# Optimization experiments

Measured on AMD Instinct MI355X. Metric: run time of the kernel, lower is better.

## Reference

```python
import jax, jax.numpy as jnp
import numpy as np

B, T, D, H = 256, 1024, 64, 128


def _orthogonal(key, shape):
    a = jax.random.normal(key, (max(shape), max(shape)), dtype=jnp.float32)
    q, _ = jnp.linalg.qr(a)
    return q[: shape[0], : shape[1]].astype(jnp.float32)


def setup_inputs() -> dict:
    key = jax.random.key(0)
    k0, k1, k2, k3 = jax.random.split(key, 4)
    x = jax.random.normal(k0, (B, T, D), dtype=jnp.float32)
    W_xK = _orthogonal(k1, (H, D))
    W_xz = _orthogonal(k2, (H, D))
    W_hK = _orthogonal(k3, (H, H))
    b_xK = jnp.zeros((H,), jnp.float32)
    b_xz = jnp.zeros((H,), jnp.float32)
    b_hK = jnp.zeros((H,), jnp.float32)
    return {"x": x, "W_xK": W_xK, "b_xK": b_xK, "W_xz": W_xz,
            "b_xz": b_xz, "W_hK": W_hK, "b_hK": b_hK}


def reference(x, W_xK, b_xK, W_xz, b_xz, W_hK, b_hK):
    # Precompute input projections for all timesteps (batched GEMM).
    gate_x_K = jnp.einsum('btd,hd->bth', x, W_xK) + b_xK  # [B,T,H]
    gate_x_z = jnp.einsum('btd,hd->bth', x, W_xz) + b_xz  # [B,T,H]
    z_all = jnp.tanh(gate_x_z)                             # [B,T,H]
    h0 = jnp.zeros((x.shape[0], W_hK.shape[0]), x.dtype)

    def step(h, inputs):
        gxK, z = inputs  # each [B,H]
        gate_h_K = h @ W_hK.T + b_hK
        K_gain = jax.nn.sigmoid(gxK + gate_h_K)
        h_new = jnp.tanh(h + K_gain * (z - h))
        return h_new, h_new

    # scan over time dim
    _, outs = jax.lax.scan(step, h0,
                           (jnp.swapaxes(gate_x_K, 0, 1),
                            jnp.swapaxes(z_all, 0, 1)))
    outs = jnp.swapaxes(outs, 0, 1)  # [B,T,H]
    return (outs, outs)
```

## Files before the change

### kernel.cpp

```cpp
#include <hip/hip_runtime.h>
#include <hip/hip_bf16.h>
#include <hip/hip_fp16.h>

#define NB 256
#define NT 1024
#define ND 64
#define NH 128

typedef __fp16 half8 __attribute__((ext_vector_type(8)));
typedef __fp16 half2v __attribute__((ext_vector_type(2)));
typedef float float4v __attribute__((ext_vector_type(4)));

#define REGION_H 262144
#define GX_OFF   131072
#define Z_BASE   67108864

static __device__ __forceinline__ float fast_tanh(float v) {
    float e = __expf(2.0f * v);
    return 1.0f - 2.0f * __builtin_amdgcn_rcpf(e + 1.0f);
}

static __device__ __forceinline__ float fdot2f(half2v a, half2v b, float c) {
#if __has_builtin(__builtin_amdgcn_fdot2)
    return __builtin_amdgcn_fdot2(a, b, c, false);
#else
    return c + (float)a.x * (float)b.x + (float)a.y * (float)b.y;
#endif
}

static __device__ __forceinline__ void fast_barrier() {
    asm volatile("s_waitcnt lgkmcnt(0)\n\ts_barrier" ::: "memory");
}

static __device__ __forceinline__ float dpp_xor1_add(float x) {
#if __has_builtin(__builtin_amdgcn_mov_dpp)
    int o = __builtin_amdgcn_mov_dpp(__builtin_bit_cast(int, x), 0xB1, 0xF, 0xF, true);
    return x + __builtin_bit_cast(float, o);
#else
    return x + __shfl_xor(x, 1);
#endif
}

__global__ __launch_bounds__(256) void proj_kernel(
        const float* __restrict__ x,
        const float* __restrict__ WxK, const float* __restrict__ bxK,
        const float* __restrict__ Wxz, const float* __restrict__ bxz,
        __fp16* __restrict__ stg) {
    __shared__ __align__(16) __fp16 wsm[2][128][72];
    __shared__ __align__(16) __fp16 xsm[64][72];
    __shared__ __align__(16) __fp16 rpk[2][64][128];

    const int tid = threadIdx.x;

    for (int mat = 0; mat < 2; ++mat) {
        const float* Wsrc = mat ? Wxz : WxK;
        const float4v* ws4 = (const float4v*)(Wsrc + (size_t)(tid >> 1) * 64 + (tid & 1) * 32);
        #pragma unroll
        for (int i = 0; i < 4; ++i) {
            float4v a = ws4[2 * i], b = ws4[2 * i + 1];
            half8 hv = {(__fp16)a.x, (__fp16)a.y, (__fp16)a.z, (__fp16)a.w,
                        (__fp16)b.x, (__fp16)b.y, (__fp16)b.z, (__fp16)b.w};
            *(half8*)&wsm[mat][tid >> 1][(tid & 1) * 32 + i * 8] = hv;
        }
    }

    const int wid = tid >> 6, lane = tid & 63;
    const int l16 = lane & 15, kg = lane >> 4;

    float bKv[8], bzv[8];
    #pragma unroll
    for (int nt = 0; nt < 8; ++nt) {
        bKv[nt] = bxK[nt * 16 + l16];
        bzv[nt] = bxz[nt * 16 + l16];
    }

    for (int sub = 0; sub < 4; ++sub) {
        const int m0 = blockIdx.x * 256 + sub * 64;
        {
            const float4v* xs4 = (const float4v*)(x + (size_t)(m0 + (tid >> 2)) * 64 + (tid & 3) * 16);
            #pragma unroll
            for (int i = 0; i < 2; ++i) {
                float4v a = xs4[2 * i], b = xs4[2 * i + 1];
                half8 hv = {(__fp16)a.x, (__fp16)a.y, (__fp16)a.z, (__fp16)a.w,
                            (__fp16)b.x, (__fp16)b.y, (__fp16)b.z, (__fp16)b.w};
                *(half8*)&xsm[tid >> 2][(tid & 3) * 16 + i * 8] = hv;
            }
        }
        __syncthreads();

        float4v acc[16] = {};
        #pragma unroll
        for (int s = 0; s < 2; ++s) {
            half8 af = *(const half8*)&xsm[wid * 16 + l16][s * 32 + kg * 8];
            #pragma unroll
            for (int nt = 0; nt < 8; ++nt) {
                #pragma unroll
                for (int mat = 0; mat < 2; ++mat) {
                    half8 bf = *(const half8*)&wsm[mat][nt * 16 + l16][s * 32 + kg * 8];
                    acc[nt * 2 + mat] =
                        __builtin_amdgcn_mfma_f32_16x16x32_f16(af, bf, acc[nt * 2 + mat], 0, 0, 0);
                }
            }
        }

        #pragma unroll
        for (int nt = 0; nt < 8; ++nt) {
            const int col = nt * 16 + l16;
            #pragma unroll
            for (int r = 0; r < 4; ++r) {
                const int row = wid * 16 + kg * 4 + r;
                rpk[0][row][col] = (__fp16)(acc[nt * 2 + 0][r] + bKv[nt]);
                rpk[1][row][col] = (__fp16)fast_tanh(acc[nt * 2 + 1][r] + bzv[nt]);
            }
        }
        __syncthreads();

        const int bb = m0 >> 10, tt0 = m0 & 1023;
        const size_t g0 = (size_t)bb * REGION_H + GX_OFF + (size_t)tt0 * NH;
        float4v* dstg = (float4v*)(stg + g0);
        float4v* dstz = (float4v*)(stg + g0 + (size_t)Z_BASE);
        const float4v* srcg = (const float4v*)rpk[0];
        const float4v* srcz = (const float4v*)rpk[1];
        #pragma unroll
        for (int i = 0; i < 4; ++i) {
            dstg[tid * 4 + i] = srcg[tid * 4 + i];
            dstz[tid * 4 + i] = srcz[tid * 4 + i];
        }
    }
}

__global__ __launch_bounds__(256) void rnn_kernel(
        const float* __restrict__ Whk, const float* __restrict__ bhk,
        float* __restrict__ out) {
    __shared__ __align__(16) __fp16 hbuf[2][128];
    __shared__ __align__(16) __fp16 gbuf[2][16][128];
    __shared__ __align__(16) __fp16 zbuf[2][16][128];

    const int tid = threadIdx.x;
    const int b = blockIdx.x;
    const int j = tid >> 1, kh = tid & 1;

    half2v w[32];
    {
        const float4v* wsrc = (const float4v*)(Whk + (size_t)j * NH + kh * 64);
        #pragma unroll
        for (int i = 0; i < 16; ++i) {
            float4v wv = wsrc[i];
            w[2 * i]     = __builtin_amdgcn_cvt_pkrtz(wv.x, wv.y);
            w[2 * i + 1] = __builtin_amdgcn_cvt_pkrtz(wv.z, wv.w);
        }
    }
    const float bj = bhk[j];

    const __fp16* gxb = (const __fp16*)out + (size_t)b * REGION_H + GX_OFF;
    const float4v* gsrc4 = (const float4v*)gxb;
    const float4v* zsrc4 = (const float4v*)(gxb + (size_t)Z_BASE);

    float4v pg = gsrc4[tid];
    float4v pz = zsrc4[tid];
    ((float4v*)gbuf[0])[tid] = pg;
    ((float4v*)zbuf[0])[tid] = pz;
    if (tid < 128) hbuf[0][tid] = (__fp16)0.0f;

    float hn = 0.0f;
    float oreg[16];
    const size_t obase = (size_t)kh * ((size_t)NB * NT * NH)
                       + (size_t)b * NT * NH + j;
    __syncthreads();

    for (int c = 0; c < 64; ++c) {
        const int cb = c & 1;

        if (c + 1 < 64) {
            pg = gsrc4[(c + 1) * 256 + tid];
            pz = zsrc4[(c + 1) * 256 + tid];
        }

        float gxv[16], zvv[16];
        #pragma unroll
        for (int s = 0; s < 16; ++s) {
            gxv[s] = (float)gbuf[cb][s][j] + bj;
            zvv[s] = (float)zbuf[cb][s][j];
        }

        #pragma unroll
        for (int s = 0; s < 16; ++s) {
            const int t = c * 16 + s;
            const half8* hs = (const half8*)&hbuf[t & 1][kh * 64];
            float a0 = 0.f, a1 = 0.f, a2 = 0.f, a3 = 0.f;
            #pragma unroll
            for (int i = 0; i < 8; ++i) {
                half8 hv = hs[i];
                a0 = fdot2f(w[4 * i + 0], __builtin_shufflevector(hv, hv, 0, 1), a0);
                a1 = fdot2f(w[4 * i + 1], __builtin_shufflevector(hv, hv, 2, 3), a1);
                a2 = fdot2f(w[4 * i + 2], __builtin_shufflevector(hv, hv, 4, 5), a2);
                a3 = fdot2f(w[4 * i + 3], __builtin_shufflevector(hv, hv, 6, 7), a3);
            }
            const float acc = (a0 + a1) + (a2 + a3);
            const float gh = dpp_xor1_add(acc);

            const float d = zvv[s] - hn;
            const float pre = gh + gxv[s];
            const float Kg = __builtin_amdgcn_rcpf(1.0f + __expf(-pre));
            const float v = __builtin_fmaf(Kg, d, hn);
            hn = fast_tanh(v);
            oreg[s] = hn;

            if (kh == 0) hbuf[(t + 1) & 1][j] = (__fp16)hn;

            if (s == 14 && c + 1 < 64) {
                ((float4v*)gbuf[cb ^ 1])[tid] = pg;
                ((float4v*)zbuf[cb ^ 1])[tid] = pz;
            }
            fast_barrier();
        }

        #pragma unroll
        for (int s = 0; s < 16; ++s)
            out[obase + (size_t)(c * 16 + s) * NH] = oreg[s];
    }
}

extern "C" void kernel_launch(void* const* d_in, const int* in_sizes, int n_in,
                              void* d_out, int out_size, void* d_ws, size_t ws_size,
                              hipStream_t stream) {
    (void)in_sizes; (void)n_in; (void)d_ws; (void)ws_size; (void)out_size;
    const float* x   = (const float*)d_in[0];
    const float* WxK = (const float*)d_in[1];
    const float* bxK = (const float*)d_in[2];
    const float* Wxz = (const float*)d_in[3];
    const float* bxz = (const float*)d_in[4];
    const float* Whk = (const float*)d_in[5];
    const float* bhk = (const float*)d_in[6];
    float* out = (float*)d_out;

    proj_kernel<<<1024, 256, 0, stream>>>(x, WxK, bxK, Wxz, bxz, (__fp16*)d_out);
    rnn_kernel<<<256, 256, 0, stream>>>(Whk, bhk, out);
}
```

Measured before the change: 603.9 us.

## Fuse input projection into recurrent kernel, computing chunk projections via MFMA in-loop

```diff
diff --git a/kernel.cpp b/kernel.cpp
--- a/kernel.cpp
+++ b/kernel.cpp
@@ -8,12 +8,9 @@
 #define NH 128
 
 typedef __fp16 half8 __attribute__((ext_vector_type(8)));
+typedef __fp16 half4v __attribute__((ext_vector_type(4)));
 typedef __fp16 half2v __attribute__((ext_vector_type(2)));
 typedef float float4v __attribute__((ext_vector_type(4)));
-
-#define REGION_H 262144
-#define GX_OFF   131072
-#define Z_BASE   67108864
 
 static __device__ __forceinline__ float fast_tanh(float v) {
     float e = __expf(2.0f * v);
@@ -41,104 +38,36 @@
 #endif
 }
 
-__global__ __launch_bounds__(256) void proj_kernel(
+__global__ __launch_bounds__(256) void fused_rnn_kernel(
         const float* __restrict__ x,
         const float* __restrict__ WxK, const float* __restrict__ bxK,
         const float* __restrict__ Wxz, const float* __restrict__ bxz,
-        __fp16* __restrict__ stg) {
+        const float* __restrict__ Whk, const float* __restrict__ bhk,
+        float* __restrict__ out) {
     __shared__ __align__(16) __fp16 wsm[2][128][72];
-    __shared__ __align__(16) __fp16 xsm[64][72];
-    __shared__ __align__(16) __fp16 rpk[2][64][128];
+    __shared__ __align__(16) __fp16 xsm[16][72];
+    __shared__ __align__(16) __fp16 hbuf[2][128];
+    __shared__ __align__(16) __fp16 gbuf[2][16][132];
+    __shared__ __align__(16) __fp16 zbuf[2][16][132];
 
     const int tid = threadIdx.x;
-
+    const int b = blockIdx.x;
+    const int wid = tid >> 6, lane = tid & 63;
+    const int l16 = lane & 15, kg = lane >> 4;
+    const int j = tid >> 1, kh = tid & 1;
+
+    #pragma unroll
     for (int mat = 0; mat < 2; ++mat) {
         const float* Wsrc = mat ? Wxz : WxK;
         const float4v* ws4 = (const float4v*)(Wsrc + (size_t)(tid >> 1) * 64 + (tid & 1) * 32);
         #pragma unroll
         for (int i = 0; i < 4; ++i) {
-            float4v a = ws4[2 * i], b = ws4[2 * i + 1];
+            float4v a = ws4[2 * i], c = ws4[2 * i + 1];
             half8 hv = {(__fp16)a.x, (__fp16)a.y, (__fp16)a.z, (__fp16)a.w,
-                        (__fp16)b.x, (__fp16)b.y, (__fp16)b.z, (__fp16)b.w};
+                        (__fp16)c.x, (__fp16)c.y, (__fp16)c.z, (__fp16)c.w};
             *(half8*)&wsm[mat][tid >> 1][(tid & 1) * 32 + i * 8] = hv;
         }
     }
-
-    const int wid = tid >> 6, lane = tid & 63;
-    const int l16 = lane & 15, kg = lane >> 4;
-
-    float bKv[8], bzv[8];
-    #pragma unroll
-    for (int nt = 0; nt < 8; ++nt) {
-        bKv[nt] = bxK[nt * 16 + l16];
-        bzv[nt] = bxz[nt * 16 + l16];
-    }
-
-    for (int sub = 0; sub < 4; ++sub) {
-        const int m0 = blockIdx.x * 256 + sub * 64;
-        {
-            const float4v* xs4 = (const float4v*)(x + (size_t)(m0 + (tid >> 2)) * 64 + (tid & 3) * 16);
-            #pragma unroll
-            for (int i = 0; i < 2; ++i) {
-                float4v a = xs4[2 * i], b = xs4[2 * i + 1];
-                half8 hv = {(__fp16)a.x, (__fp16)a.y, (__fp16)a.z, (__fp16)a.w,
-                            (__fp16)b.x, (__fp16)b.y, (__fp16)b.z, (__fp16)b.w};
-                *(half8*)&xsm[tid >> 2][(tid & 3) * 16 + i * 8] = hv;
-            }
-        }
-        __syncthreads();
-
-        float4v acc[16] = {};
-        #pragma unroll
-        for (int s = 0; s < 2; ++s) {
-            half8 af = *(const half8*)&xsm[wid * 16 + l16][s * 32 + kg * 8];
-            #pragma unroll
-            for (int nt = 0; nt < 8; ++nt) {
-                #pragma unroll
-                for (int mat = 0; mat < 2; ++mat) {
-                    half8 bf = *(const half8*)&wsm[mat][nt * 16 + l16][s * 32 + kg * 8];
-                    acc[nt * 2 + mat] =
-                        __builtin_amdgcn_mfma_f32_16x16x32_f16(af, bf, acc[nt * 2 + mat], 0, 0, 0);
-                }
-            }
-        }
-
-        #pragma unroll
-        for (int nt = 0; nt < 8; ++nt) {
-            const int col = nt * 16 + l16;
-            #pragma unroll
-            for (int r = 0; r < 4; ++r) {
-                const int row = wid * 16 + kg * 4 + r;
-                rpk[0][row][col] = (__fp16)(acc[nt * 2 + 0][r] + bKv[nt]);
-                rpk[1][row][col] = (__fp16)fast_tanh(acc[nt * 2 + 1][r] + bzv[nt]);
-            }
-        }
-        __syncthreads();
-
-        const int bb = m0 >> 10, tt0 = m0 & 1023;
-        const size_t g0 = (size_t)bb * REGION_H + GX_OFF + (size_t)tt0 * NH;
-        float4v* dstg = (float4v*)(stg + g0);
-        float4v* dstz = (float4v*)(stg + g0 + (size_t)Z_BASE);
-        const float4v* srcg = (const float4v*)rpk[0];
-        const float4v* srcz = (const float4v*)rpk[1];
-        #pragma unroll
-        for (int i = 0; i < 4; ++i) {
-            dstg[tid * 4 + i] = srcg[tid * 4 + i];
-            dstz[tid * 4 + i] = srcz[tid * 4 + i];
-        }
-    }
-}
-
-__global__ __launch_bounds__(256) void rnn_kernel(
-        const float* __restrict__ Whk, const float* __restrict__ bhk,
-        float* __restrict__ out) {
-    __shared__ __align__(16) __fp16 hbuf[2][128];
-    __shared__ __align__(16) __fp16 gbuf[2][16][128];
-    __shared__ __align__(16) __fp16 zbuf[2][16][128];
-
-    const int tid = threadIdx.x;
-    const int b = blockIdx.x;
-    const int j = tid >> 1, kh = tid & 1;
 
     half2v w[32];
     {
@@ -152,29 +81,73 @@
     }
     const float bj = bhk[j];
 
-    const __fp16* gxb = (const __fp16*)out + (size_t)b * REGION_H + GX_OFF;
-    const float4v* gsrc4 = (const float4v*)gxb;
-    const float4v* zsrc4 = (const float4v*)(gxb + (size_t)Z_BASE);
-
-    float4v pg = gsrc4[tid];
-    float4v pz = zsrc4[tid];
-    ((float4v*)gbuf[0])[tid] = pg;
-    ((float4v*)zbuf[0])[tid] = pz;
-    if (tid < 128) hbuf[0][tid] = (__fp16)0.0f;
+    const int hc0 = (2 * wid + 0) * 16 + l16;
+    const int hc1 = (2 * wid + 1) * 16 + l16;
+    const float bK0 = bxK[hc0], bK1 = bxK[hc1];
+    const float bz0 = bxz[hc0], bz1 = bxz[hc1];
+
+    const float4v* xsrc = (const float4v*)(x + (size_t)b * NT * ND);
+
+    auto proj_mfma = [&](float4v (&pacc)[2][2]) {
+        #pragma unroll
+        for (int n2 = 0; n2 < 2; ++n2)
+            #pragma unroll
+            for (int mat = 0; mat < 2; ++mat)
+                pacc[n2][mat] = (float4v){0.f, 0.f, 0.f, 0.f};
+        #pragma unroll
+        for (int ks = 0; ks < 2; ++ks) {
+            half8 af = *(const half8*)&xsm[l16][ks * 32 + kg * 8];
+            #pragma unroll
+            for (int n2 = 0; n2 < 2; ++n2) {
+                const int nt = 2 * wid + n2;
+                #pragma unroll
+                for (int mat = 0; mat < 2; ++mat) {
+                    half8 bf = *(const half8*)&wsm[mat][nt * 16 + l16][ks * 32 + kg * 8];
+                    pacc[n2][mat] =
+                        __builtin_amdgcn_mfma_f32_16x16x32_f16(af, bf, pacc[n2][mat], 0, 0, 0);
+                }
+            }
+        }
+    };
+    auto proj_epilogue = [&](float4v (&pacc)[2][2], int dst) {
+        #pragma unroll
+        for (int n2 = 0; n2 < 2; ++n2) {
+            const int col = (2 * wid + n2) * 16 + l16;
+            const float bK = n2 ? bK1 : bK0;
+            const float bz = n2 ? bz1 : bz0;
+            #pragma unroll
+            for (int r = 0; r < 4; ++r) {
+                const int row = kg * 4 + r;
+                gbuf[dst][row][col] = (__fp16)(pacc[n2][0][r] + bK);
+                zbuf[dst][row][col] = (__fp16)fast_tanh(pacc[n2][1][r] + bz);
+            }
+        }
+    };
+
+    {
+        float4v xg = xsrc[tid];
+        if (tid < 128) hbuf[0][tid] = (__fp16)0.0f;
+        __syncthreads();
+        half4v hx = {(__fp16)xg.x, (__fp16)xg.y, (__fp16)xg.z, (__fp16)xg.w};
+        *(half4v*)&xsm[tid >> 4][(tid & 15) * 4] = hx;
+        __syncthreads();
+        float4v pacc[2][2];
+        proj_mfma(pacc);
+        proj_epilogue(pacc, 0);
+        __syncthreads();
+    }
 
     float hn = 0.0f;
     float oreg[16];
     const size_t obase = (size_t)kh * ((size_t)NB * NT * NH)
                        + (size_t)b * NT * NH + j;
-    __syncthreads();
 
     for (int c = 0; c < 64; ++c) {
         const int cb = c & 1;
-
-        if (c + 1 < 64) {
-            pg = gsrc4[(c + 1) * 256 + tid];
-            pz = zsrc4[(c + 1) * 256 + tid];
-        }
+        const bool more = (c + 1 < 64);
+
+        float4v xgn;
+        if (more) xgn = xsrc[(c + 1) * 256 + tid];
 
         float gxv[16], zvv[16];
         #pragma unroll
@@ -182,6 +155,8 @@
             gxv[s] = (float)gbuf[cb][s][j] + bj;
             zvv[s] = (float)zbuf[cb][s][j];
         }
+
+        float4v pacc[2][2];
 
         #pragma unroll
         for (int s = 0; s < 16; ++s) {
@@ -208,10 +183,13 @@
 
             if (kh == 0) hbuf[(t + 1) & 1][j] = (__fp16)hn;
 
-            if (s == 14 && c + 1 < 64) {
-                ((float4v*)gbuf[cb ^ 1])[tid] = pg;
-                ((float4v*)zbuf[cb ^ 1])[tid] = pz;
-            }
+            if (s == 2 && more) {
+                half4v hx = {(__fp16)xgn.x, (__fp16)xgn.y, (__fp16)xgn.z, (__fp16)xgn.w};
+                *(half4v*)&xsm[tid >> 4][(tid & 15) * 4] = hx;
+            }
+            if (s == 4 && more) proj_mfma(pacc);
+            if (s == 6 && more) proj_epilogue(pacc, cb ^ 1);
+
             fast_barrier();
         }
 
@@ -234,6 +212,5 @@
     const float* bhk = (const float*)d_in[6];
     float* out = (float*)d_out;
 
-    proj_kernel<<<1024, 256, 0, stream>>>(x, WxK, bxK, Wxz, bxz, (__fp16*)d_out);
-    rnn_kernel<<<256, 256, 0, stream>>>(Whk, bhk, out);
-}
+    fused_rnn_kernel<<<256, 256, 0, stream>>>(x, WxK, bxK, Wxz, bxz, Whk, bhk, out);
+}
```

Result: faster. 584.3 us (-3.2%).
